# Optimization experiments

Measured on AMD Instinct MI355X. Metric: run time of the kernel, lower is better.

## Reference

```python
import jax, jax.numpy as jnp
import numpy as np

HID, HEADS, HD = 512, 8, 64  # hid_dim, n_heads, head_dim
NEG = -1e10


def setup_inputs() -> dict:
    key = jax.random.key(0)
    ks = jax.random.split(key, 12)
    B, S = 4, 2048
    inp = {
        'query': jax.random.normal(ks[0], (B, S, HID), jnp.float32),
        'key': jax.random.normal(ks[1], (B, S, HID), jnp.float32),
        'value': jax.random.normal(ks[2], (B, S, HID), jnp.float32),
        'mask': jnp.ones((B, 1, 1, S), jnp.int32),
    }
    sc = 1.0 / np.sqrt(HID)
    for i, n in enumerate(['Wq', 'Wk', 'Wv', 'Wo']):
        inp[n] = jax.random.uniform(ks[3 + i], (HID, HID), jnp.float32, -sc, sc)
    for i, n in enumerate(['bq', 'bk', 'bv', 'bo']):
        inp[n] = jax.random.uniform(ks[7 + i], (HID,), jnp.float32, -sc, sc)
    return inp


def reference(query, key, value, mask, Wq, Wk, Wv, Wo, bq, bk, bv, bo):
    B = query.shape[0]

    def proj(x, W, b):
        # torch Linear: x @ W.T + b; then split heads -> [B, H, S, HD]
        y = jnp.einsum('bsd,ed->bse', x, W) + b
        return y.reshape(B, -1, HEADS, HD).transpose(0, 2, 1, 3)

    Q = proj(query, Wq, bq)
    K = proj(key, Wk, bk)
    V = proj(value, Wv, bv)
    scale = jnp.sqrt(jnp.float32(HD))
    E = jnp.einsum('bhqd,bhkd->bhqk', Q, K) / scale  # [B,H,Sq,Sk]
    E = jnp.where(mask == 0, NEG, E)
    A = jax.nn.softmax(E, axis=-1)  # dropout p=0 -> identity
    out = jnp.einsum('bhqk,bhkd->bhqd', A, V)
    out = out.transpose(0, 2, 1, 3).reshape(B, -1, HID)
    return jnp.einsum('bsd,ed->bse', out, Wo) + bo
```

## Files before the change

kernel.cpp:

```cpp
#include <hip/hip_runtime.h>
#include <hip/hip_bf16.h>


typedef __bf16 v8bf __attribute__((ext_vector_type(8)));
typedef __bf16 v4bf __attribute__((ext_vector_type(4)));
typedef float  v4f  __attribute__((ext_vector_type(4)));

#define MFMA16(a, b, c) __builtin_amdgcn_mfma_f32_16x16x32_bf16((a), (b), (c), 0, 0, 0)

__device__ __forceinline__ void gl16(const __bf16* g, __bf16* l) {
    __builtin_amdgcn_global_load_lds(
        (const __attribute__((address_space(1))) void*)g,
        (__attribute__((address_space(3))) void*)l, 16, 0, 0);
}

__device__ inline v8bf cvt8(const float* __restrict__ p) {
    const v4f f0 = *(const v4f*)p;
    const v4f f1 = *(const v4f*)(p + 4);
    v8bf r;
    r[0] = (__bf16)f0[0]; r[1] = (__bf16)f0[1]; r[2] = (__bf16)f0[2]; r[3] = (__bf16)f0[3];
    r[4] = (__bf16)f1[0]; r[5] = (__bf16)f1[1]; r[6] = (__bf16)f1[2]; r[7] = (__bf16)f1[3];
    return r;
}

__global__ __launch_bounds__(256) void cvt_all(
    const float* __restrict__ Wq, const float* __restrict__ Wk,
    const float* __restrict__ Wv, const float* __restrict__ Wo,
    const float* __restrict__ xq, const float* __restrict__ xk,
    const float* __restrict__ xv,
    __bf16* __restrict__ Wb, __bf16* __restrict__ xb)
{
    const int bid = blockIdx.x;
    if (bid < 1024) {
        const int idx = (bid * 256 + threadIdx.x) * 4;
        const int w = idx >> 18, off = idx & 262143;
        const float* src = (w == 0) ? Wq : (w == 1) ? Wk : (w == 2) ? Wv : Wo;
        const v4f x = *(const v4f*)(src + off);
        v4bf y;
        y[0] = (__bf16)x[0]; y[1] = (__bf16)x[1]; y[2] = (__bf16)x[2]; y[3] = (__bf16)x[3];
        *(v4bf*)(Wb + idx) = y;
    } else {
        const int idx = ((bid - 1024) * 256 + threadIdx.x) * 8;
        const int w = idx >> 22, off = idx & 4194303;
        const float* src = (w == 0) ? xq : (w == 1) ? xk : xv;
        *(v8bf*)(xb + idx) = cvt8(src + off);
    }
}

__global__ __launch_bounds__(256) void qkv_gemm(
    const __bf16* __restrict__ xb, const __bf16* __restrict__ Wb,
    const float* __restrict__ bq, const float* __restrict__ bk, const float* __restrict__ bv,
    __bf16* __restrict__ Qo, __bf16* __restrict__ Ko, __bf16* __restrict__ VTo)
{
    const int z = blockIdx.z;
    const __bf16* x    = xb + (size_t)z * 4194304;
    const __bf16* W    = Wb + (size_t)z * 262144;
    const float*  bias = (z == 0) ? bq : (z == 1) ? bk : bv;

    const int tid = threadIdx.x, wave = tid >> 6, lane = tid & 63;
    const int quad = lane >> 4, r = lane & 15;
    const int wm = wave >> 1, wn = wave & 1;
    const int row0 = blockIdx.x * 128, col0 = blockIdx.y * 128;

    __shared__ __align__(16) __bf16 As[2][4096];
    __shared__ __align__(16) __bf16 Bs[2][4096];

    const __bf16* aG[2];
    const __bf16* bG[2];
    int aOff[2];
    for (int j = 0; j < 2; j++) {
        const int s = wave * 2 + j;
        aG[j] = x + (size_t)(row0 + s * 16 + r) * 512 + quad * 8;
        bG[j] = W + (size_t)(col0 + s * 16 + r) * 512 + quad * 8;
        aOff[j] = s * 512;
    }

    v4f acc[4][4] = {};

    for (int j = 0; j < 2; j++) {
        gl16(aG[j], &As[0][aOff[j]]);
        gl16(bG[j], &Bs[0][aOff[j]]);
    }
    __syncthreads();

    for (int t = 0; t < 16; t++) {
        const int cur = t & 1;
        if (t < 15) {
            const int kk = (t + 1) * 32;
            for (int j = 0; j < 2; j++) {
                gl16(aG[j] + kk, &As[cur ^ 1][aOff[j]]);
                gl16(bG[j] + kk, &Bs[cur ^ 1][aOff[j]]);
            }
        }
        v8bf a[4], b[4];
        for (int i = 0; i < 4; i++)
            a[i] = ((const v8bf*)As[cur])[(wm * 4 + i) * 64 + lane];
        for (int i = 0; i < 4; i++)
            b[i] = ((const v8bf*)Bs[cur])[(wn * 4 + i) * 64 + lane];
        for (int mi = 0; mi < 4; mi++)
            for (int ni = 0; ni < 4; ni++)
                acc[mi][ni] = MFMA16(a[mi], b[ni], acc[mi][ni]);
        __syncthreads();
    }

    for (int ni = 0; ni < 4; ni++) {
        const int n = col0 + wn * 64 + ni * 16 + r;
        const float bv_ = bias[n];
        const int hh = n >> 6, hd = n & 63;
        for (int mi = 0; mi < 4; mi++) {
            const int mbase = row0 + wm * 64 + mi * 16 + quad * 4;
            const int bb = mbase >> 11, s0 = mbase & 2047;
            if (z == 2) {
                v4bf pk;
                for (int i = 0; i < 4; i++)
                    pk[i] = (__bf16)(acc[mi][ni][i] + bv_);
                *(v4bf*)&VTo[((size_t)((bb * 8 + hh) * 64 + hd)) * 2048 + s0] = pk;
            } else {
                __bf16* dst = (z == 0) ? Qo : Ko;
                for (int i = 0; i < 4; i++)
                    dst[((size_t)((bb * 8 + hh) * 2048 + s0 + i)) * 64 + hd] =
                        (__bf16)(acc[mi][ni][i] + bv_);
            }
        }
    }
}

__global__ __launch_bounds__(256, 2) void attn(
    const __bf16* __restrict__ Q, const __bf16* __restrict__ K,
    const __bf16* __restrict__ VT, const int* __restrict__ mask,
    __bf16* __restrict__ AO)
{
    const int id = blockIdx.y * 16 + blockIdx.x;
    const int x8 = id & 7, j = (id >> 3) & 3, qb = id >> 5;
    const int bh = x8 * 4 + j;
    const int b = bh >> 3, h = bh & 7;
    const int tid = threadIdx.x, wave = tid >> 6, lane = tid & 63;
    const int quad = lane >> 4, r = lane & 15;
    const int q0 = qb * 128 + wave * 32;

    const __bf16* Qb = Q  + (size_t)bh * 2048 * 64;
    const __bf16* Kb = K  + (size_t)bh * 2048 * 64;
    const __bf16* Vb = VT + (size_t)bh * 64 * 2048;
    const int*    mb = mask + (size_t)b * 2048;

    __shared__ __align__(16) __bf16 Kls[2][4096];
    __shared__ __align__(16) __bf16 Vls[2][4096];
    __shared__ __align__(16) float  biasF[2048];
    __shared__ __align__(16) __bf16 PF[4][4][64][8];

    for (int i = tid; i < 2048; i += 256)
        biasF[i] = (mb[i] != 0) ? 0.f : -1.0e10f;

    const int e1 = tid, e2 = tid + 256;
    int seg, l, t_, h_, rr, qd;
    seg = e1 >> 6; l = e1 & 63; t_ = seg >> 1; h_ = seg & 1; rr = l & 15; qd = l >> 4;
    const __bf16* kg1 = Kb + (size_t)(16 * t_ + rr) * 64   + h_ * 32 + qd * 8;
    const __bf16* vg1 = Vb + (size_t)(16 * t_ + rr) * 2048 + h_ * 32 + qd * 8;
    seg = e2 >> 6; l = e2 & 63; t_ = seg >> 1; h_ = seg & 1; rr = l & 15; qd = l >> 4;
    const __bf16* kg2 = Kb + (size_t)(16 * t_ + rr) * 64   + h_ * 32 + qd * 8;
    const __bf16* vg2 = Vb + (size_t)(16 * t_ + rr) * 2048 + h_ * 32 + qd * 8;

    v8bf qf[2][2];
    for (int g = 0; g < 2; g++) {
        qf[g][0] = *(const v8bf*)(Qb + (size_t)(q0 + g * 16 + r) * 64 +      quad * 8);
        qf[g][1] = *(const v8bf*)(Qb + (size_t)(q0 + g * 16 + r) * 64 + 32 + quad * 8);
    }

    v8bf ones;
    for (int i = 0; i < 8; i++) ones[i] = (__bf16)1.0f;

    v4f o[2][4] = {};
    v4f osum[2] = {};

    const float SC = 0.18033688f;

    const int entE = (quad >> 1) * 16 + r;
    const int entO = entE + 32;
    const int eoff = (quad & 1) * 4;

    v8bf ks1 = *(const v8bf*)kg1, ks2 = *(const v8bf*)kg2;
    v8bf vs1 = *(const v8bf*)vg1, vs2 = *(const v8bf*)vg2;
    ((v8bf*)Kls[0])[e1] = ks1; ((v8bf*)Kls[0])[e2] = ks2;
    ((v8bf*)Vls[0])[e1] = vs1; ((v8bf*)Vls[0])[e2] = vs2;
    ks1 = *(const v8bf*)(kg1 + (size_t)64 * 64);
    ks2 = *(const v8bf*)(kg2 + (size_t)64 * 64);
    vs1 = *(const v8bf*)(vg1 + 64);
    vs2 = *(const v8bf*)(vg2 + 64);
    __syncthreads();

    int cur = 0;
    for (int t = 0; t < 32; t++) {
        const int k0 = t * 64;

        v4f sa[2][4] = {};
        for (int tt = 0; tt < 4; tt++) {
            const v8bf kf0 = ((const v8bf*)Kls[cur])[(tt * 2 + 0) * 64 + lane];
            const v8bf kf1 = ((const v8bf*)Kls[cur])[(tt * 2 + 1) * 64 + lane];
            sa[0][tt] = MFMA16(kf0, qf[0][0], sa[0][tt]);
            sa[0][tt] = MFMA16(kf1, qf[0][1], sa[0][tt]);
            sa[1][tt] = MFMA16(kf0, qf[1][0], sa[1][tt]);
            sa[1][tt] = MFMA16(kf1, qf[1][1], sa[1][tt]);
        }

        for (int tt = 0; tt < 4; tt++) {
            const v4f bl = *(const v4f*)&biasF[k0 + tt * 16 + quad * 4];
            const int ent = (tt & 1) ? entO : entE;
            const int pl = tt >> 1;
            for (int g = 0; g < 2; g++) {
                v4bf pk;
                for (int i = 0; i < 4; i++) {
                    const float p = __builtin_amdgcn_exp2f(fmaf(sa[g][tt][i], SC, bl[i]));
                    pk[i] = (__bf16)p;
                }
                *(v4bf*)&PF[wave][g * 2 + pl][ent][eoff] = pk;
            }
        }
        asm volatile("s_waitcnt lgkmcnt(0)" ::: "memory");
        v8bf pa[2][2];
        for (int g = 0; g < 2; g++) {
            pa[g][0] = *(const v8bf*)&PF[wave][g * 2 + 0][lane][0];
            pa[g][1] = *(const v8bf*)&PF[wave][g * 2 + 1][lane][0];
        }

        osum[0] = MFMA16(pa[0][0], ones, osum[0]);
        osum[0] = MFMA16(pa[0][1], ones, osum[0]);
        osum[1] = MFMA16(pa[1][0], ones, osum[1]);
        osum[1] = MFMA16(pa[1][1], ones, osum[1]);

        for (int t2 = 0; t2 < 4; t2++) {
            const v8bf vf0 = ((const v8bf*)Vls[cur])[(t2 * 2 + 0) * 64 + lane];
            const v8bf vf1 = ((const v8bf*)Vls[cur])[(t2 * 2 + 1) * 64 + lane];
            o[0][t2] = MFMA16(pa[0][0], vf0, o[0][t2]);
            o[0][t2] = MFMA16(pa[0][1], vf1, o[0][t2]);
            o[1][t2] = MFMA16(pa[1][0], vf0, o[1][t2]);
            o[1][t2] = MFMA16(pa[1][1], vf1, o[1][t2]);
        }

        if (t < 31) {
            ((v8bf*)Kls[cur ^ 1])[e1] = ks1; ((v8bf*)Kls[cur ^ 1])[e2] = ks2;
            ((v8bf*)Vls[cur ^ 1])[e1] = vs1; ((v8bf*)Vls[cur ^ 1])[e2] = vs2;
            if (t < 30) {
                const int k0n = (t + 2) * 64;
                ks1 = *(const v8bf*)(kg1 + (size_t)k0n * 64);
                ks2 = *(const v8bf*)(kg2 + (size_t)k0n * 64);
                vs1 = *(const v8bf*)(vg1 + k0n);
                vs2 = *(const v8bf*)(vg2 + k0n);
            }
        }
        __syncthreads();
        cur ^= 1;
    }

    for (int g = 0; g < 2; g++) {
        float inv[4];
        for (int i = 0; i < 4; i++) inv[i] = 1.0f / osum[g][i];
        for (int t2 = 0; t2 < 4; t2++) {
            const int hd = t2 * 16 + r;
            for (int i = 0; i < 4; i++) {
                const int s = q0 + g * 16 + quad * 4 + i;
                AO[((size_t)b * 2048 + s) * 512 + h * 64 + hd] =
                    (__bf16)(o[g][t2][i] * inv[i]);
            }
        }
    }
}

__global__ __launch_bounds__(256) void out_gemm(
    const __bf16* __restrict__ Ai, const __bf16* __restrict__ W,
    const float* __restrict__ bias, float* __restrict__ y)
{
    const int tid = threadIdx.x, wave = tid >> 6, lane = tid & 63;
    const int quad = lane >> 4, r = lane & 15;
    const int wm = wave >> 1, wn = wave & 1;
    const int row0 = blockIdx.x * 64, col0 = blockIdx.y * 128;

    __shared__ __align__(16) __bf16 As[2][2048];
    __shared__ __align__(16) __bf16 Bs[2][4096];

    const __bf16* aG = Ai + (size_t)(row0 + wave * 16 + r) * 512 + quad * 8;
    const int aOff = wave * 512;
    const __bf16* bG[2];
    int bOff[2];
    for (int j = 0; j < 2; j++) {
        const int s = wave * 2 + j;
        bG[j] = W + (size_t)(col0 + s * 16 + r) * 512 + quad * 8;
        bOff[j] = s * 512;
    }

    v4f acc[2][4] = {};

    gl16(aG, &As[0][aOff]);
    gl16(bG[0], &Bs[0][bOff[0]]);
    gl16(bG[1], &Bs[0][bOff[1]]);
    __syncthreads();

    for (int t = 0; t < 16; t++) {
        const int cur = t & 1;
        if (t < 15) {
            const int kk = (t + 1) * 32;
            gl16(aG + kk, &As[cur ^ 1][aOff]);
            gl16(bG[0] + kk, &Bs[cur ^ 1][bOff[0]]);
            gl16(bG[1] + kk, &Bs[cur ^ 1][bOff[1]]);
        }
        v8bf a[2], b[4];
        for (int i = 0; i < 2; i++)
            a[i] = ((const v8bf*)As[cur])[(wm * 2 + i) * 64 + lane];
        for (int i = 0; i < 4; i++)
            b[i] = ((const v8bf*)Bs[cur])[(wn * 4 + i) * 64 + lane];
        for (int mi = 0; mi < 2; mi++)
            for (int ni = 0; ni < 4; ni++)
                acc[mi][ni] = MFMA16(a[mi], b[ni], acc[mi][ni]);
        __syncthreads();
    }

    for (int ni = 0; ni < 4; ni++) {
        const int n = col0 + wn * 64 + ni * 16 + r;
        const float bv_ = bias[n];
        for (int mi = 0; mi < 2; mi++) {
            const int mbase = row0 + wm * 32 + mi * 16 + quad * 4;
            for (int i = 0; i < 4; i++)
                y[(size_t)(mbase + i) * 512 + n] = acc[mi][ni][i] + bv_;
        }
    }
}

extern "C" void kernel_launch(void* const* d_in, const int* in_sizes, int n_in,
                              void* d_out, int out_size, void* d_ws, size_t ws_size,
                              hipStream_t stream)
{
    const float* q    = (const float*)d_in[0];
    const float* k    = (const float*)d_in[1];
    const float* v    = (const float*)d_in[2];
    const int*   mask = (const int*)d_in[3];
    const float* Wq   = (const float*)d_in[4];
    const float* Wk   = (const float*)d_in[5];
    const float* Wv   = (const float*)d_in[6];
    const float* Wo   = (const float*)d_in[7];
    const float* bq   = (const float*)d_in[8];
    const float* bk   = (const float*)d_in[9];
    const float* bv   = (const float*)d_in[10];
    const float* bo   = (const float*)d_in[11];

    __bf16* ws  = (__bf16*)d_ws;
    __bf16* Qw  = ws;
    __bf16* Kw  = ws + 4194304;
    __bf16* VTw = ws + 8388608;
    __bf16* AOw = ws + 12582912;
    __bf16* Wb  = ws + 16777216;
    __bf16* xbw = ws + 17825792;

    cvt_all<<<dim3(7168), 256, 0, stream>>>(Wq, Wk, Wv, Wo, q, k, v, Wb, xbw);
    qkv_gemm<<<dim3(64, 4, 3), 256, 0, stream>>>(xbw, Wb, bq, bk, bv, Qw, Kw, VTw);
    attn<<<dim3(16, 32), 256, 0, stream>>>(Qw, Kw, VTw, mask, AOw);
    out_gemm<<<dim3(128, 4), 256, 0, stream>>>(AOw, Wb + 786432, bo, (float*)d_out);
}
```

Baseline: 207.2 us.

## Fuse fp32-to-bf16 activation conversion into QKV GEMM A-operand loads

```diff
diff --git a/kernel.cpp b/kernel.cpp
--- a/kernel.cpp
+++ b/kernel.cpp
@@ -14,46 +14,35 @@
         (__attribute__((address_space(3))) void*)l, 16, 0, 0);
 }
 
-__device__ inline v8bf cvt8(const float* __restrict__ p) {
-    const v4f f0 = *(const v4f*)p;
-    const v4f f1 = *(const v4f*)(p + 4);
+__device__ __forceinline__ v8bf cvt8v(const v4f f0, const v4f f1) {
     v8bf r;
     r[0] = (__bf16)f0[0]; r[1] = (__bf16)f0[1]; r[2] = (__bf16)f0[2]; r[3] = (__bf16)f0[3];
     r[4] = (__bf16)f1[0]; r[5] = (__bf16)f1[1]; r[6] = (__bf16)f1[2]; r[7] = (__bf16)f1[3];
     return r;
 }
 
-__global__ __launch_bounds__(256) void cvt_all(
+__global__ __launch_bounds__(256) void cvt_w(
     const float* __restrict__ Wq, const float* __restrict__ Wk,
     const float* __restrict__ Wv, const float* __restrict__ Wo,
+    __bf16* __restrict__ out)
+{
+    const int idx = (blockIdx.x * 256 + threadIdx.x) * 4;
+    const int w = idx >> 18, off = idx & 262143;
+    const float* src = (w == 0) ? Wq : (w == 1) ? Wk : (w == 2) ? Wv : Wo;
+    const v4f x = *(const v4f*)(src + off);
+    v4bf y;
+    y[0] = (__bf16)x[0]; y[1] = (__bf16)x[1]; y[2] = (__bf16)x[2]; y[3] = (__bf16)x[3];
+    *(v4bf*)(out + idx) = y;
+}
+
+__global__ __launch_bounds__(256, 3) void qkv_gemm(
     const float* __restrict__ xq, const float* __restrict__ xk,
-    const float* __restrict__ xv,
-    __bf16* __restrict__ Wb, __bf16* __restrict__ xb)
-{
-    const int bid = blockIdx.x;
-    if (bid < 1024) {
-        const int idx = (bid * 256 + threadIdx.x) * 4;
-        const int w = idx >> 18, off = idx & 262143;
-        const float* src = (w == 0) ? Wq : (w == 1) ? Wk : (w == 2) ? Wv : Wo;
-        const v4f x = *(const v4f*)(src + off);
-        v4bf y;
-        y[0] = (__bf16)x[0]; y[1] = (__bf16)x[1]; y[2] = (__bf16)x[2]; y[3] = (__bf16)x[3];
-        *(v4bf*)(Wb + idx) = y;
-    } else {
-        const int idx = ((bid - 1024) * 256 + threadIdx.x) * 8;
-        const int w = idx >> 22, off = idx & 4194303;
-        const float* src = (w == 0) ? xq : (w == 1) ? xk : xv;
-        *(v8bf*)(xb + idx) = cvt8(src + off);
-    }
-}
-
-__global__ __launch_bounds__(256) void qkv_gemm(
-    const __bf16* __restrict__ xb, const __bf16* __restrict__ Wb,
+    const float* __restrict__ xv, const __bf16* __restrict__ Wb,
     const float* __restrict__ bq, const float* __restrict__ bk, const float* __restrict__ bv,
     __bf16* __restrict__ Qo, __bf16* __restrict__ Ko, __bf16* __restrict__ VTo)
 {
     const int z = blockIdx.z;
-    const __bf16* x    = xb + (size_t)z * 4194304;
+    const float*  x    = (z == 0) ? xq : (z == 1) ? xk : xv;
     const __bf16* W    = Wb + (size_t)z * 262144;
     const float*  bias = (z == 0) ? bq : (z == 1) ? bk : bv;
 
@@ -62,39 +51,46 @@
     const int wm = wave >> 1, wn = wave & 1;
     const int row0 = blockIdx.x * 128, col0 = blockIdx.y * 128;
 
-    __shared__ __align__(16) __bf16 As[2][4096];
     __shared__ __align__(16) __bf16 Bs[2][4096];
 
-    const __bf16* aG[2];
+    const float* aP[4];
+    for (int i = 0; i < 4; i++)
+        aP[i] = x + (size_t)(row0 + (wm * 4 + i) * 16 + r) * 512 + quad * 8;
+
     const __bf16* bG[2];
-    int aOff[2];
+    int bOff[2];
     for (int j = 0; j < 2; j++) {
         const int s = wave * 2 + j;
-        aG[j] = x + (size_t)(row0 + s * 16 + r) * 512 + quad * 8;
         bG[j] = W + (size_t)(col0 + s * 16 + r) * 512 + quad * 8;
-        aOff[j] = s * 512;
+        bOff[j] = s * 512;
     }
 
     v4f acc[4][4] = {};
-
-    for (int j = 0; j < 2; j++) {
-        gl16(aG[j], &As[0][aOff[j]]);
-        gl16(bG[j], &Bs[0][aOff[j]]);
-    }
+    v4f aF[4][2];
+
+    for (int i = 0; i < 4; i++) {
+        aF[i][0] = *(const v4f*)(aP[i]);
+        aF[i][1] = *(const v4f*)(aP[i] + 4);
+    }
+    gl16(bG[0], &Bs[0][bOff[0]]);
+    gl16(bG[1], &Bs[0][bOff[1]]);
     __syncthreads();
 
     for (int t = 0; t < 16; t++) {
         const int cur = t & 1;
+        v8bf a[4];
+        for (int i = 0; i < 4; i++)
+            a[i] = cvt8v(aF[i][0], aF[i][1]);
         if (t < 15) {
             const int kk = (t + 1) * 32;
-            for (int j = 0; j < 2; j++) {
-                gl16(aG[j] + kk, &As[cur ^ 1][aOff[j]]);
-                gl16(bG[j] + kk, &Bs[cur ^ 1][aOff[j]]);
-            }
-        }
-        v8bf a[4], b[4];
-        for (int i = 0; i < 4; i++)
-            a[i] = ((const v8bf*)As[cur])[(wm * 4 + i) * 64 + lane];
+            for (int i = 0; i < 4; i++) {
+                aF[i][0] = *(const v4f*)(aP[i] + kk);
+                aF[i][1] = *(const v4f*)(aP[i] + kk + 4);
+            }
+            gl16(bG[0] + kk, &Bs[cur ^ 1][bOff[0]]);
+            gl16(bG[1] + kk, &Bs[cur ^ 1][bOff[1]]);
+        }
+        v8bf b[4];
         for (int i = 0; i < 4; i++)
             b[i] = ((const v8bf*)Bs[cur])[(wn * 4 + i) * 64 + lane];
         for (int mi = 0; mi < 4; mi++)
@@ -347,10 +343,9 @@
     __bf16* VTw = ws + 8388608;
     __bf16* AOw = ws + 12582912;
     __bf16* Wb  = ws + 16777216;
-    __bf16* xbw = ws + 17825792;
-
-    cvt_all<<<dim3(7168), 256, 0, stream>>>(Wq, Wk, Wv, Wo, q, k, v, Wb, xbw);
-    qkv_gemm<<<dim3(64, 4, 3), 256, 0, stream>>>(xbw, Wb, bq, bk, bv, Qw, Kw, VTw);
+
+    cvt_w<<<dim3(1024), 256, 0, stream>>>(Wq, Wk, Wv, Wo, Wb);
+    qkv_gemm<<<dim3(64, 4, 3), 256, 0, stream>>>(q, k, v, Wb, bq, bk, bv, Qw, Kw, VTw);
     attn<<<dim3(16, 32), 256, 0, stream>>>(Qw, Kw, VTw, mask, AOw);
     out_gemm<<<dim3(128, 4), 256, 0, stream>>>(AOw, Wb + 786432, bo, (float*)d_out);
 }
```

After: 229.3 us. 10.7% more time.

## Split attention over key halves with fp32 partials and a combine kernel

Applied to the files above, without the earlier changes.

```diff
diff --git a/kernel.cpp b/kernel.cpp
--- a/kernel.cpp
+++ b/kernel.cpp
@@ -125,30 +125,34 @@
     }
 }
 
-__global__ __launch_bounds__(256, 2) void attn(
+__global__ __launch_bounds__(256, 4) void attn(
     const __bf16* __restrict__ Q, const __bf16* __restrict__ K,
     const __bf16* __restrict__ VT, const int* __restrict__ mask,
-    __bf16* __restrict__ AO)
+    float* __restrict__ P0, float* __restrict__ P1,
+    float* __restrict__ L0, float* __restrict__ L1)
 {
     const int id = blockIdx.y * 16 + blockIdx.x;
     const int x8 = id & 7, j = (id >> 3) & 3, qb = id >> 5;
     const int bh = x8 * 4 + j;
     const int b = bh >> 3, h = bh & 7;
+    const int ks = blockIdx.z;
+    float* __restrict__ Pp = ks ? P1 : P0;
+    float* __restrict__ Lp = ks ? L1 : L0;
     const int tid = threadIdx.x, wave = tid >> 6, lane = tid & 63;
     const int quad = lane >> 4, r = lane & 15;
     const int q0 = qb * 128 + wave * 32;
 
     const __bf16* Qb = Q  + (size_t)bh * 2048 * 64;
-    const __bf16* Kb = K  + (size_t)bh * 2048 * 64;
-    const __bf16* Vb = VT + (size_t)bh * 64 * 2048;
-    const int*    mb = mask + (size_t)b * 2048;
-
-    __shared__ __align__(16) __bf16 Kls[2][4096];
-    __shared__ __align__(16) __bf16 Vls[2][4096];
-    __shared__ __align__(16) float  biasF[2048];
+    const __bf16* Kb = K  + (size_t)bh * 2048 * 64 + (size_t)ks * 1024 * 64;
+    const __bf16* Vb = VT + (size_t)bh * 64 * 2048 + ks * 1024;
+    const int*    mb = mask + (size_t)b * 2048 + ks * 1024;
+
+    __shared__ __align__(16) __bf16 Kls[4096];
+    __shared__ __align__(16) __bf16 Vls[4096];
+    __shared__ __align__(16) float  biasF[1024];
     __shared__ __align__(16) __bf16 PF[4][4][64][8];
 
-    for (int i = tid; i < 2048; i += 256)
+    for (int i = tid; i < 1024; i += 256)
         biasF[i] = (mb[i] != 0) ? 0.f : -1.0e10f;
 
     const int e1 = tid, e2 = tid + 256;
@@ -180,22 +184,25 @@
 
     v8bf ks1 = *(const v8bf*)kg1, ks2 = *(const v8bf*)kg2;
     v8bf vs1 = *(const v8bf*)vg1, vs2 = *(const v8bf*)vg2;
-    ((v8bf*)Kls[0])[e1] = ks1; ((v8bf*)Kls[0])[e2] = ks2;
-    ((v8bf*)Vls[0])[e1] = vs1; ((v8bf*)Vls[0])[e2] = vs2;
-    ks1 = *(const v8bf*)(kg1 + (size_t)64 * 64);
-    ks2 = *(const v8bf*)(kg2 + (size_t)64 * 64);
-    vs1 = *(const v8bf*)(vg1 + 64);
-    vs2 = *(const v8bf*)(vg2 + 64);
-    __syncthreads();
-
-    int cur = 0;
-    for (int t = 0; t < 32; t++) {
+
+    for (int t = 0; t < 16; t++) {
+        __syncthreads();
+        ((v8bf*)Kls)[e1] = ks1; ((v8bf*)Kls)[e2] = ks2;
+        ((v8bf*)Vls)[e1] = vs1; ((v8bf*)Vls)[e2] = vs2;
+        __syncthreads();
+        if (t < 15) {
+            const int k0n = (t + 1) * 64;
+            ks1 = *(const v8bf*)(kg1 + (size_t)k0n * 64);
+            ks2 = *(const v8bf*)(kg2 + (size_t)k0n * 64);
+            vs1 = *(const v8bf*)(vg1 + k0n);
+            vs2 = *(const v8bf*)(vg2 + k0n);
+        }
         const int k0 = t * 64;
 
         v4f sa[2][4] = {};
         for (int tt = 0; tt < 4; tt++) {
-            const v8bf kf0 = ((const v8bf*)Kls[cur])[(tt * 2 + 0) * 64 + lane];
-            const v8bf kf1 = ((const v8bf*)Kls[cur])[(tt * 2 + 1) * 64 + lane];
+            const v8bf kf0 = ((const v8bf*)Kls)[(tt * 2 + 0) * 64 + lane];
+            const v8bf kf1 = ((const v8bf*)Kls)[(tt * 2 + 1) * 64 + lane];
             sa[0][tt] = MFMA16(kf0, qf[0][0], sa[0][tt]);
             sa[0][tt] = MFMA16(kf1, qf[0][1], sa[0][tt]);
             sa[1][tt] = MFMA16(kf0, qf[1][0], sa[1][tt]);
@@ -228,41 +235,47 @@
         osum[1] = MFMA16(pa[1][1], ones, osum[1]);
 
         for (int t2 = 0; t2 < 4; t2++) {
-            const v8bf vf0 = ((const v8bf*)Vls[cur])[(t2 * 2 + 0) * 64 + lane];
-            const v8bf vf1 = ((const v8bf*)Vls[cur])[(t2 * 2 + 1) * 64 + lane];
+            const v8bf vf0 = ((const v8bf*)Vls)[(t2 * 2 + 0) * 64 + lane];
+            const v8bf vf1 = ((const v8bf*)Vls)[(t2 * 2 + 1) * 64 + lane];
             o[0][t2] = MFMA16(pa[0][0], vf0, o[0][t2]);
             o[0][t2] = MFMA16(pa[0][1], vf1, o[0][t2]);
             o[1][t2] = MFMA16(pa[1][0], vf0, o[1][t2]);
             o[1][t2] = MFMA16(pa[1][1], vf1, o[1][t2]);
         }
-
-        if (t < 31) {
-            ((v8bf*)Kls[cur ^ 1])[e1] = ks1; ((v8bf*)Kls[cur ^ 1])[e2] = ks2;
-            ((v8bf*)Vls[cur ^ 1])[e1] = vs1; ((v8bf*)Vls[cur ^ 1])[e2] = vs2;
-            if (t < 30) {
-                const int k0n = (t + 2) * 64;
-                ks1 = *(const v8bf*)(kg1 + (size_t)k0n * 64);
-                ks2 = *(const v8bf*)(kg2 + (size_t)k0n * 64);
-                vs1 = *(const v8bf*)(vg1 + k0n);
-                vs2 = *(const v8bf*)(vg2 + k0n);
-            }
-        }
-        __syncthreads();
-        cur ^= 1;
     }
 
     for (int g = 0; g < 2; g++) {
-        float inv[4];
-        for (int i = 0; i < 4; i++) inv[i] = 1.0f / osum[g][i];
+        if (r == 0)
+            for (int i = 0; i < 4; i++)
+                Lp[(size_t)bh * 2048 + q0 + g * 16 + quad * 4 + i] = osum[g][i];
         for (int t2 = 0; t2 < 4; t2++) {
             const int hd = t2 * 16 + r;
             for (int i = 0; i < 4; i++) {
                 const int s = q0 + g * 16 + quad * 4 + i;
-                AO[((size_t)b * 2048 + s) * 512 + h * 64 + hd] =
-                    (__bf16)(o[g][t2][i] * inv[i]);
+                Pp[((size_t)b * 2048 + s) * 512 + h * 64 + hd] = o[g][t2][i];
             }
         }
     }
+}
+
+__global__ __launch_bounds__(256) void combine(
+    const float* __restrict__ P0, const float* __restrict__ P1,
+    const float* __restrict__ L0, const float* __restrict__ L1,
+    __bf16* __restrict__ AO)
+{
+    const size_t idx = ((size_t)blockIdx.x * 256 + threadIdx.x) * 8;
+    const int bb = (int)(idx >> 20);
+    const int rem = (int)(idx & 1048575);
+    const int s = rem >> 9;
+    const int h = (rem & 511) >> 6;
+    const size_t li = ((size_t)bb * 8 + h) * 2048 + s;
+    const float inv = 1.0f / (L0[li] + L1[li]);
+    const v4f a0 = *(const v4f*)(P0 + idx), a1 = *(const v4f*)(P0 + idx + 4);
+    const v4f b0 = *(const v4f*)(P1 + idx), b1 = *(const v4f*)(P1 + idx + 4);
+    v8bf r;
+    for (int i = 0; i < 4; i++) r[i]     = (__bf16)((a0[i] + b0[i]) * inv);
+    for (int i = 0; i < 4; i++) r[i + 4] = (__bf16)((a1[i] + b1[i]) * inv);
+    *(v8bf*)(AO + idx) = r;
 }
 
 __global__ __launch_bounds__(256) void out_gemm(
@@ -345,12 +358,17 @@
     __bf16* Qw  = ws;
     __bf16* Kw  = ws + 4194304;
     __bf16* VTw = ws + 8388608;
-    __bf16* AOw = ws + 12582912;
-    __bf16* Wb  = ws + 16777216;
-    __bf16* xbw = ws + 17825792;
+    __bf16* Wb  = ws + 12582912;
+    __bf16* xbw = ws + 13631488;
+    float*  P0  = (float*)(ws + 13631488);
+    float*  P1  = (float*)(ws + 22020096);
+    float*  L0  = (float*)(ws + 30408704);
+    float*  L1  = (float*)(ws + 30539776);
+    __bf16* AOw = Qw;
 
     cvt_all<<<dim3(7168), 256, 0, stream>>>(Wq, Wk, Wv, Wo, q, k, v, Wb, xbw);
     qkv_gemm<<<dim3(64, 4, 3), 256, 0, stream>>>(xbw, Wb, bq, bk, bv, Qw, Kw, VTw);
-    attn<<<dim3(16, 32), 256, 0, stream>>>(Qw, Kw, VTw, mask, AOw);
+    attn<<<dim3(16, 32, 2), 256, 0, stream>>>(Qw, Kw, VTw, mask, P0, P1, L0, L1);
+    combine<<<dim3(2048), 256, 0, stream>>>(P0, P1, L0, L1, AOw);
     out_gemm<<<dim3(128, 4), 256, 0, stream>>>(AOw, Wb + 786432, bo, (float*)d_out);
 }
```

Measured after the change: 208.1 us. No clear change (+0.4%).

## Split attention key range across two wave groups per block and merge partials

Applied to the files above, without the earlier changes.

```diff
diff --git a/kernel.cpp b/kernel.cpp
--- a/kernel.cpp
+++ b/kernel.cpp
@@ -125,7 +125,7 @@
     }
 }
 
-__global__ __launch_bounds__(256, 2) void attn(
+__global__ __launch_bounds__(512, 4) void attn(
     const __bf16* __restrict__ Q, const __bf16* __restrict__ K,
     const __bf16* __restrict__ VT, const int* __restrict__ mask,
     __bf16* __restrict__ AO)
@@ -135,23 +135,26 @@
     const int bh = x8 * 4 + j;
     const int b = bh >> 3, h = bh & 7;
     const int tid = threadIdx.x, wave = tid >> 6, lane = tid & 63;
+    const int w4 = wave & 3, half = wave >> 2;
+    const int ltid = tid & 255;
     const int quad = lane >> 4, r = lane & 15;
-    const int q0 = qb * 128 + wave * 32;
+    const int q0 = qb * 128 + w4 * 32;
 
     const __bf16* Qb = Q  + (size_t)bh * 2048 * 64;
-    const __bf16* Kb = K  + (size_t)bh * 2048 * 64;
-    const __bf16* Vb = VT + (size_t)bh * 64 * 2048;
+    const __bf16* Kb = K  + (size_t)bh * 2048 * 64 + (size_t)half * 1024 * 64;
+    const __bf16* Vb = VT + (size_t)bh * 64 * 2048 + half * 1024;
     const int*    mb = mask + (size_t)b * 2048;
 
     __shared__ __align__(16) __bf16 Kls[2][4096];
     __shared__ __align__(16) __bf16 Vls[2][4096];
     __shared__ __align__(16) float  biasF[2048];
-    __shared__ __align__(16) __bf16 PF[4][4][64][8];
-
-    for (int i = tid; i < 2048; i += 256)
+    __shared__ __align__(16) __bf16 PF[8][4][64][8];
+    __shared__ float osumX[4][32];
+
+    for (int i = tid; i < 2048; i += 512)
         biasF[i] = (mb[i] != 0) ? 0.f : -1.0e10f;
 
-    const int e1 = tid, e2 = tid + 256;
+    const int e1 = ltid, e2 = ltid + 256;
     int seg, l, t_, h_, rr, qd;
     seg = e1 >> 6; l = e1 & 63; t_ = seg >> 1; h_ = seg & 1; rr = l & 15; qd = l >> 4;
     const __bf16* kg1 = Kb + (size_t)(16 * t_ + rr) * 64   + h_ * 32 + qd * 8;
@@ -180,22 +183,25 @@
 
     v8bf ks1 = *(const v8bf*)kg1, ks2 = *(const v8bf*)kg2;
     v8bf vs1 = *(const v8bf*)vg1, vs2 = *(const v8bf*)vg2;
-    ((v8bf*)Kls[0])[e1] = ks1; ((v8bf*)Kls[0])[e2] = ks2;
-    ((v8bf*)Vls[0])[e1] = vs1; ((v8bf*)Vls[0])[e2] = vs2;
-    ks1 = *(const v8bf*)(kg1 + (size_t)64 * 64);
-    ks2 = *(const v8bf*)(kg2 + (size_t)64 * 64);
-    vs1 = *(const v8bf*)(vg1 + 64);
-    vs2 = *(const v8bf*)(vg2 + 64);
-    __syncthreads();
-
-    int cur = 0;
-    for (int t = 0; t < 32; t++) {
+
+    for (int t = 0; t < 16; t++) {
+        __syncthreads();
+        ((v8bf*)Kls[half])[e1] = ks1; ((v8bf*)Kls[half])[e2] = ks2;
+        ((v8bf*)Vls[half])[e1] = vs1; ((v8bf*)Vls[half])[e2] = vs2;
+        __syncthreads();
+        if (t < 15) {
+            const int k0n = (t + 1) * 64;
+            ks1 = *(const v8bf*)(kg1 + (size_t)k0n * 64);
+            ks2 = *(const v8bf*)(kg2 + (size_t)k0n * 64);
+            vs1 = *(const v8bf*)(vg1 + k0n);
+            vs2 = *(const v8bf*)(vg2 + k0n);
+        }
         const int k0 = t * 64;
 
         v4f sa[2][4] = {};
         for (int tt = 0; tt < 4; tt++) {
-            const v8bf kf0 = ((const v8bf*)Kls[cur])[(tt * 2 + 0) * 64 + lane];
-            const v8bf kf1 = ((const v8bf*)Kls[cur])[(tt * 2 + 1) * 64 + lane];
+            const v8bf kf0 = ((const v8bf*)Kls[half])[(tt * 2 + 0) * 64 + lane];
+            const v8bf kf1 = ((const v8bf*)Kls[half])[(tt * 2 + 1) * 64 + lane];
             sa[0][tt] = MFMA16(kf0, qf[0][0], sa[0][tt]);
             sa[0][tt] = MFMA16(kf1, qf[0][1], sa[0][tt]);
             sa[1][tt] = MFMA16(kf0, qf[1][0], sa[1][tt]);
@@ -203,7 +209,7 @@
         }
 
         for (int tt = 0; tt < 4; tt++) {
-            const v4f bl = *(const v4f*)&biasF[k0 + tt * 16 + quad * 4];
+            const v4f bl = *(const v4f*)&biasF[half * 1024 + k0 + tt * 16 + quad * 4];
             const int ent = (tt & 1) ? entO : entE;
             const int pl = tt >> 1;
             for (int g = 0; g < 2; g++) {
@@ -228,38 +234,43 @@
         osum[1] = MFMA16(pa[1][1], ones, osum[1]);
 
         for (int t2 = 0; t2 < 4; t2++) {
-            const v8bf vf0 = ((const v8bf*)Vls[cur])[(t2 * 2 + 0) * 64 + lane];
-            const v8bf vf1 = ((const v8bf*)Vls[cur])[(t2 * 2 + 1) * 64 + lane];
+            const v8bf vf0 = ((const v8bf*)Vls[half])[(t2 * 2 + 0) * 64 + lane];
+            const v8bf vf1 = ((const v8bf*)Vls[half])[(t2 * 2 + 1) * 64 + lane];
             o[0][t2] = MFMA16(pa[0][0], vf0, o[0][t2]);
             o[0][t2] = MFMA16(pa[0][1], vf1, o[0][t2]);
             o[1][t2] = MFMA16(pa[1][0], vf0, o[1][t2]);
             o[1][t2] = MFMA16(pa[1][1], vf1, o[1][t2]);
         }
-
-        if (t < 31) {
-            ((v8bf*)Kls[cur ^ 1])[e1] = ks1; ((v8bf*)Kls[cur ^ 1])[e2] = ks2;
-            ((v8bf*)Vls[cur ^ 1])[e1] = vs1; ((v8bf*)Vls[cur ^ 1])[e2] = vs2;
-            if (t < 30) {
-                const int k0n = (t + 2) * 64;
-                ks1 = *(const v8bf*)(kg1 + (size_t)k0n * 64);
-                ks2 = *(const v8bf*)(kg2 + (size_t)k0n * 64);
-                vs1 = *(const v8bf*)(vg1 + k0n);
-                vs2 = *(const v8bf*)(vg2 + k0n);
-            }
-        }
-        __syncthreads();
-        cur ^= 1;
-    }
-
-    for (int g = 0; g < 2; g++) {
-        float inv[4];
-        for (int i = 0; i < 4; i++) inv[i] = 1.0f / osum[g][i];
-        for (int t2 = 0; t2 < 4; t2++) {
-            const int hd = t2 * 16 + r;
-            for (int i = 0; i < 4; i++) {
-                const int s = q0 + g * 16 + quad * 4 + i;
-                AO[((size_t)b * 2048 + s) * 512 + h * 64 + hd] =
-                    (__bf16)(o[g][t2][i] * inv[i]);
+    }
+
+    __syncthreads();
+    float* ex = (float*)&PF[0][0][0][0];
+    if (half == 1) {
+        for (int g = 0; g < 2; g++) {
+            for (int t2 = 0; t2 < 4; t2++)
+                for (int i = 0; i < 4; i++)
+                    ex[(w4 * 32 + g * 16 + quad * 4 + i) * 64 + t2 * 16 + r] =
+                        o[g][t2][i];
+            if (r == 0)
+                for (int i = 0; i < 4; i++)
+                    osumX[w4][g * 16 + quad * 4 + i] = osum[g][i];
+        }
+    }
+    __syncthreads();
+    if (half == 0) {
+        for (int g = 0; g < 2; g++) {
+            float inv[4];
+            for (int i = 0; i < 4; i++)
+                inv[i] = 1.0f / (osum[g][i] + osumX[w4][g * 16 + quad * 4 + i]);
+            for (int t2 = 0; t2 < 4; t2++) {
+                const int hd = t2 * 16 + r;
+                for (int i = 0; i < 4; i++) {
+                    const int s = q0 + g * 16 + quad * 4 + i;
+                    const float val = o[g][t2][i] +
+                        ex[(w4 * 32 + g * 16 + quad * 4 + i) * 64 + hd];
+                    AO[((size_t)b * 2048 + s) * 512 + h * 64 + hd] =
+                        (__bf16)(val * inv[i]);
+                }
             }
         }
     }
@@ -351,6 +362,6 @@
 
     cvt_all<<<dim3(7168), 256, 0, stream>>>(Wq, Wk, Wv, Wo, q, k, v, Wb, xbw);
     qkv_gemm<<<dim3(64, 4, 3), 256, 0, stream>>>(xbw, Wb, bq, bk, bv, Qw, Kw, VTw);
-    attn<<<dim3(16, 32), 256, 0, stream>>>(Qw, Kw, VTw, mask, AOw);
+    attn<<<dim3(16, 32), 512, 0, stream>>>(Qw, Kw, VTw, mask, AOw);
     out_gemm<<<dim3(128, 4), 256, 0, stream>>>(AOw, Wb + 786432, bo, (float*)d_out);
 }
```

Result: faster. 201.2 us, median of 3 (-2.9%).
